# Optimization experiments

Hardware: AMD Instinct MI355X
Metric: run time of the kernel (lower is better)

## Reference

```python
import jax, jax.numpy as jnp
import numpy as np

TOP_RATIO = 0.7
MIN_PATCHES = 128
RANDOM_RATIO = 0.1


def setup_inputs() -> dict:
    key = jax.random.key(0)
    k1, k2, k3, k4 = jax.random.split(key, 4)
    B, N, D, H = 4, 16384, 512, 256
    features = jax.random.normal(k1, (B, N, D), dtype=jnp.float32)
    W_V = jax.random.normal(k2, (D, H), dtype=jnp.float32) * (1.0 / np.sqrt(D))
    W_U = jax.random.normal(k3, (D, H), dtype=jnp.float32) * (1.0 / np.sqrt(D))
    w_att = jax.random.normal(k4, (H,), dtype=jnp.float32) * (1.0 / np.sqrt(H))
    return {
        "features": features,
        "W_V": W_V, "b_V": jnp.zeros((H,), jnp.float32),
        "W_U": W_U, "b_U": jnp.zeros((H,), jnp.float32),
        "w_att": w_att, "b_att": jnp.zeros((), jnp.float32),
    }


def reference(features, W_V, b_V, W_U, b_U, w_att, b_att):
    B, N, D = features.shape
    # gated attention scoring (dropout disabled: eval mode)
    a_V = jnp.tanh(features @ W_V + b_V)              # (B, N, H)
    a_U = jax.nn.sigmoid(features @ W_U + b_U)        # (B, N, H)
    raw = (a_V * a_U) @ w_att + b_att                 # (B, N)
    attn = jax.nn.softmax(raw, axis=-1)               # (B, N)

    # static selection sizes
    k = min(max(int(N * TOP_RATIO), MIN_PATCHES), N)  # 11468
    n_rand = max(int(k * RANDOM_RATIO), 1)            # 1146
    n_top = k - n_rand                                # 10322

    # batched top-k (softmax is monotone in raw, same indices as torch.topk(attn))
    _, top_idx = jax.lax.top_k(attn, n_top)           # (B, n_top)

    # remaining = indices not in top_idx, ascending; fixed count N - n_top
    mask = jnp.ones((B, N), bool).at[jnp.arange(B)[:, None], top_idx].set(False)
    remaining = jnp.argsort(~mask, axis=-1, stable=True)[:, : N - n_top]  # (B, N-n_top)

    # uniform random sample of n_rand remaining indices per batch element
    scores = jax.random.uniform(jax.random.key(42), (B, N - n_top))
    perm = jnp.argsort(scores, axis=-1)[:, :n_rand]   # random n_rand positions
    rand_idx = jnp.take_along_axis(remaining, perm, axis=-1)  # (B, n_rand)

    sel_idx = jnp.sort(jnp.concatenate([top_idx, rand_idx], axis=-1), axis=-1)  # (B, k)
    selected = jnp.take_along_axis(features, sel_idx[:, :, None], axis=1)       # (B, k, D)
    return selected, attn, sel_idx
```

## Files before the change

kernel.cpp:

```cpp
#include <hip/hip_runtime.h>
#include <stdint.h>

#define B 4
#define N 16384
#define D 512
#define H 256
#define NROWS (B * N)
#define K_SEL 11468
#define N_TOP 10322
#define N_RAND 1146
#define N_REM (N - N_TOP)
#define HALF_CNT ((B * N_REM) / 2)

typedef float f32x4 __attribute__((ext_vector_type(4)));
typedef _Float16 f16x8 __attribute__((ext_vector_type(8)));
typedef int i32x4 __attribute__((ext_vector_type(4)));

#define GLDS16(g, l)                                                    \
  __builtin_amdgcn_global_load_lds(                                     \
      (const __attribute__((address_space(1))) void*)(const void*)(g),  \
      (__attribute__((address_space(3))) void*)(void*)(l), 16, 0, 0)

__device__ __forceinline__ uint32_t f2key(float x) {
  uint32_t u = __float_as_uint(x);
  return u ^ ((u & 0x80000000u) ? 0xFFFFFFFFu : 0x80000000u);
}

__device__ __forceinline__ void threefry(uint32_t x0, uint32_t x1,
                                         uint32_t& o0, uint32_t& o1) {
  const uint32_t k0 = 0u, k1 = 42u;
  const uint32_t ks[3] = {k0, k1, k0 ^ k1 ^ 0x1BD11BDAu};
  x0 += ks[0];
  x1 += ks[1];
  const int R0[4] = {13, 15, 26, 6}, R1[4] = {17, 29, 16, 24};
#pragma unroll
  for (int i = 0; i < 5; ++i) {
    const int* R = (i & 1) ? R1 : R0;
#pragma unroll
    for (int jr = 0; jr < 4; ++jr) {
      x0 += x1;
      x1 = (x1 << R[jr]) | (x1 >> (32 - R[jr]));
      x1 ^= x0;
    }
    x0 += ks[(i + 1) % 3];
    x1 += ks[(i + 2) % 3] + (uint32_t)(i + 1);
  }
  o0 = x0;
  o1 = x1;
}

__device__ __forceinline__ void rand_body(const int b, int* __restrict__ psel,
                                          char* smem, const int t) {
  uint32_t* skey = reinterpret_cast<uint32_t*>(smem);
  uint32_t* hist = reinterpret_cast<uint32_t*>(smem + 24248);
  int* wr4 = reinterpret_cast<int*>(smem + 25272);
  uint32_t* shp = reinterpret_cast<uint32_t*>(smem + 25288);
  int* shrk = reinterpret_cast<int*>(smem + 25292);
  const int lane = t & 63, w4 = t >> 6;

  for (int p = t; p < N_REM; p += 256) {
    psel[b * N_REM + p] = 0;
    const int f = b * N_REM + p;
    uint32_t o0, o1, bits;
    if (f < HALF_CNT) {
      threefry((uint32_t)f, (uint32_t)(f + HALF_CNT), o0, o1);
      bits = o0;
    } else {
      threefry((uint32_t)(f - HALF_CNT), (uint32_t)f, o0, o1);
      bits = o1;
    }
    const float u = __uint_as_float((bits >> 9) | 0x3f800000u) - 1.0f;
    skey[p] = f2key(u);
  }
  __syncthreads();

  uint32_t prefix = 0;
  int rk = N_RAND;
  for (int pass = 3; pass >= 0; --pass) {
    const int sh = pass * 8;
    hist[t] = 0;
    __syncthreads();
    for (int p = t; p < N_REM; p += 256) {
      const uint32_t key = skey[p];
      if (pass == 3 || (key >> (sh + 8)) == (prefix >> (sh + 8)))
        atomicAdd(&hist[(key >> sh) & 255], 1u);
    }
    __syncthreads();
    const int h = (int)hist[t];
    int v = h;
#pragma unroll
    for (int off = 1; off < 64; off <<= 1) {
      const int u2 = __shfl_up(v, off, 64);
      if (lane >= off) v += u2;
    }
    if (lane == 63) wr4[w4] = v;
    __syncthreads();
    int add = 0;
    for (int i = 0; i < w4; ++i) add += wr4[i];
    const int incl = v + add, excl = incl - h;
    if (incl >= rk && excl < rk) {
      *shp = prefix | ((uint32_t)t << sh);
      *shrk = rk - excl;
    }
    __syncthreads();
    prefix = *shp;
    rk = *shrk;
    __syncthreads();
  }

  const int CH = 24;
  const int p0 = t * CH;
  const int pe = (p0 + CH < N_REM) ? p0 + CH : N_REM;
  int ce = 0;
  for (int p = p0; p < pe; ++p) ce += (skey[p] == prefix);
  int v = ce;
#pragma unroll
  for (int off = 1; off < 64; off <<= 1) {
    const int u2 = __shfl_up(v, off, 64);
    if (lane >= off) v += u2;
  }
  if (lane == 63) wr4[w4] = v;
  __syncthreads();
  if (t == 0) {
    int run = 0;
    for (int i = 0; i < 4; ++i) {
      const int a = wr4[i];
      wr4[i] = run;
      run += a;
    }
  }
  __syncthreads();
  int ge = wr4[w4] + v - ce;
  for (int p = p0; p < pe; ++p) {
    const uint32_t key = skey[p];
    const bool pick = (key < prefix) || (key == prefix && ge < rk);
    ge += (key == prefix);
    if (pick) psel[b * N_REM + p] = 1;
  }
}

__global__ __launch_bounds__(256) void prep_kernel(
    const float* __restrict__ WV, const float* __restrict__ WU,
    _Float16* __restrict__ wt_h, _Float16* __restrict__ wt_l,
    int* __restrict__ psel) {
  __shared__ __align__(16) char pmem[25296];
  if (blockIdx.x >= 64) {
    rand_body(blockIdx.x - 64, psel, pmem, threadIdx.x);
    return;
  }
  _Float16(*th)[65] = reinterpret_cast<_Float16(*)[65]>(pmem);
  _Float16(*tl)[65] = reinterpret_cast<_Float16(*)[65]>(pmem + 8320);
  const int kb = (blockIdx.x >> 3) * 64;
  const int nb = (blockIdx.x & 7) * 64;
  const int tx = threadIdx.x & 63;
  const int ty = threadIdx.x >> 6;
  const float* src = (nb < 256) ? WV : WU;
  const int nsrc = nb & 255;
#pragma unroll
  for (int i = 0; i < 16; ++i) {
    const int k = ty + i * 4;
    const float x = src[(size_t)(kb + k) * H + nsrc + tx];
    const _Float16 h = (_Float16)x;
    th[k][tx] = h;
    tl[k][tx] = (_Float16)(x - (float)h);
  }
  __syncthreads();
  const int n_local = threadIdx.x & 63;
  const int c2 = threadIdx.x >> 6;
  const int s_local = c2 >> 1, half = c2 & 1;
  const int n = nb + n_local;
  const int s = (kb >> 5) + s_local;
  const int klb = s_local * 32 + half * 16;
  const int swz = (n_local >> 1) & 3;
  f16x8 vh0, vh1, vl0, vl1;
#pragma unroll
  for (int e = 0; e < 8; ++e) {
    vh0[e] = th[klb + e][n_local];
    vh1[e] = th[klb + 8 + e][n_local];
    vl0[e] = tl[klb + e][n_local];
    vl1[e] = tl[klb + 8 + e][n_local];
  }
  const size_t orow = (size_t)s * 16384 + (size_t)n * 32;
  *reinterpret_cast<f16x8*>(wt_h + orow + (((2 * half) ^ swz) * 8)) = vh0;
  *reinterpret_cast<f16x8*>(wt_h + orow + (((2 * half + 1) ^ swz) * 8)) = vh1;
  *reinterpret_cast<f16x8*>(wt_l + orow + (((2 * half) ^ swz) * 8)) = vl0;
  *reinterpret_cast<f16x8*>(wt_l + orow + (((2 * half + 1) ^ swz) * 8)) = vl1;
}

__global__ __launch_bounds__(512) void score_kernel(
    const float* __restrict__ feat, const _Float16* __restrict__ wt_h,
    const _Float16* __restrict__ wt_l, const float* __restrict__ bV,
    const float* __restrict__ bU, const float* __restrict__ watt,
    float* __restrict__ raw) {
  __shared__ _Float16 Ah[128 * 32];
  __shared__ _Float16 Al[128 * 32];
  __shared__ _Float16 Bh0[512 * 32];
  __shared__ _Float16 Bl0[512 * 32];
  __shared__ _Float16 Bh1[512 * 32];
  __shared__ _Float16 Bl1[512 * 32];
  __shared__ float red[128][5];

  const int tid = threadIdx.x;
  const int lane = tid & 63;
  const int lc = lane & 15;
  const int lg = lane >> 4;
  const int w = __builtin_amdgcn_readfirstlane(tid >> 6);
  const int rg = w >> 2;
  const int cg = w & 3;
  const int row0 = blockIdx.x * 128;

  const int rA = tid >> 2;
  const int gA = tid & 3;
  const float* aG = feat + (size_t)(row0 + rA) * D + gA * 8;
  const int awOff = rA * 32 + ((gA ^ ((rA >> 1) & 3)) << 3);

  const _Float16* pbh = wt_h + (size_t)w * 2048 + lane * 8;
  const _Float16* pbl = wt_l + (size_t)w * 2048 + lane * 8;
  const int ldsB = w * 2048;

  const int rswz = (lc >> 1) & 3;
  int aoff[4], boff[8];
#pragma unroll
  for (int mt = 0; mt < 4; ++mt)
    aoff[mt] = (rg * 64 + mt * 16 + lc) * 32 + ((lg ^ rswz) << 3);
#pragma unroll
  for (int nt = 0; nt < 8; ++nt) {
    const int nbase =
        (nt < 4) ? cg * 64 + nt * 16 : 256 + cg * 64 + (nt - 4) * 16;
    boff[nt] = (nbase + lc) * 32 + ((lg ^ rswz) << 3);
  }

  f32x4 acc[4][8] = {};
  f32x4 a0, a1;

  a0 = *(const f32x4*)(aG);
  a1 = *(const f32x4*)(aG + 4);
#pragma unroll
  for (int i = 0; i < 4; ++i) {
    GLDS16(pbh + i * 512, &Bh0[ldsB + i * 512]);
    GLDS16(pbl + i * 512, &Bl0[ldsB + i * 512]);
  }
  {
    f16x8 ahw, alw;
#pragma unroll
    for (int e = 0; e < 8; ++e) {
      const float x = (e < 4) ? a0[e] : a1[e - 4];
      const _Float16 h = (_Float16)x;
      ahw[e] = h;
      alw[e] = (_Float16)(x - (float)h);
    }
    *(f16x8*)&Ah[awOff] = ahw;
    *(f16x8*)&Al[awOff] = alw;
  }
  __syncthreads();

#pragma unroll 1
  for (int kt = 0; kt < 16; ++kt) {
    const int knx = (kt + 1) & 15;
    _Float16* BhN = (kt & 1) ? Bh0 : Bh1;
    _Float16* BlN = (kt & 1) ? Bl0 : Bl1;
    const _Float16* BhC = (kt & 1) ? Bh1 : Bh0;
    const _Float16* BlC = (kt & 1) ? Bl1 : Bl0;

#pragma unroll
    for (int i = 0; i < 4; ++i) {
      GLDS16(pbh + knx * 16384 + i * 512, &BhN[ldsB + i * 512]);
      GLDS16(pbl + knx * 16384 + i * 512, &BlN[ldsB + i * 512]);
    }
    a0 = *(const f32x4*)(aG + knx * 32);
    a1 = *(const f32x4*)(aG + knx * 32 + 4);
    __builtin_amdgcn_sched_barrier(0);

    f16x8 ah[4], al[4];
#pragma unroll
    for (int mt = 0; mt < 4; ++mt) {
      ah[mt] = *(const f16x8*)&Ah[aoff[mt]];
      al[mt] = *(const f16x8*)&Al[aoff[mt]];
    }
    f16x8 bh = *(const f16x8*)&BhC[boff[0]];
    f16x8 bl = *(const f16x8*)&BlC[boff[0]];
    __builtin_amdgcn_s_setprio(1);
#pragma unroll
    for (int nt = 0; nt < 8; ++nt) {
      f16x8 bhn, bln;
      if (nt < 7) {
        bhn = *(const f16x8*)&BhC[boff[nt + 1]];
        bln = *(const f16x8*)&BlC[boff[nt + 1]];
      }
#pragma unroll
      for (int mt = 0; mt < 4; ++mt) {
        acc[mt][nt] = __builtin_amdgcn_mfma_f32_16x16x32_f16(ah[mt], bh,
                                                             acc[mt][nt], 0, 0, 0);
        acc[mt][nt] = __builtin_amdgcn_mfma_f32_16x16x32_f16(ah[mt], bl,
                                                             acc[mt][nt], 0, 0, 0);
        acc[mt][nt] = __builtin_amdgcn_mfma_f32_16x16x32_f16(al[mt], bh,
                                                             acc[mt][nt], 0, 0, 0);
      }
      bh = bhn;
      bl = bln;
    }
    __builtin_amdgcn_s_setprio(0);

    f16x8 ahw, alw;
#pragma unroll
    for (int e = 0; e < 8; ++e) {
      const float x = (e < 4) ? a0[e] : a1[e - 4];
      const _Float16 h = (_Float16)x;
      ahw[e] = h;
      alw[e] = (_Float16)(x - (float)h);
    }
    __syncthreads();
    *(f16x8*)&Ah[awOff] = ahw;
    *(f16x8*)&Al[awOff] = alw;
    __syncthreads();
  }

#pragma unroll
  for (int mt = 0; mt < 4; ++mt) {
    float rs[4] = {0.f, 0.f, 0.f, 0.f};
#pragma unroll
    for (int nt = 0; nt < 4; ++nt) {
      const int j = cg * 64 + nt * 16 + lc;
      const float bv = bV[j], bu = bU[j], wa = watt[j];
#pragma unroll
      for (int rr = 0; rr < 4; ++rr) {
        const float cV = acc[mt][nt][rr] + bv;
        const float cU = acc[mt][nt + 4][rr] + bu;
        const float e2 = __expf(2.0f * cV);
        const float aV = 1.0f - 2.0f / (e2 + 1.0f);
        const float aU = 1.0f / (1.0f + __expf(-cU));
        rs[rr] += aV * aU * wa;
      }
    }
#pragma unroll
    for (int rr = 0; rr < 4; ++rr) {
      float v = rs[rr];
      v += __shfl_xor(v, 1, 16);
      v += __shfl_xor(v, 2, 16);
      v += __shfl_xor(v, 4, 16);
      v += __shfl_xor(v, 8, 16);
      if (lc == 0) red[rg * 64 + mt * 16 + lg * 4 + rr][cg] = v;
    }
  }
  __syncthreads();
  if (tid < 128)
    raw[row0 + tid] = red[tid][0] + red[tid][1] + red[tid][2] + red[tid][3];
}

__device__ __forceinline__ int scan1024(int c, int* wred, int tid) {
  const int lane = tid & 63, w = tid >> 6;
  int v = c;
#pragma unroll
  for (int off = 1; off < 64; off <<= 1) {
    const int u = __shfl_up(v, off, 64);
    if (lane >= off) v += u;
  }
  if (lane == 63) wred[w] = v;
  __syncthreads();
  if (tid == 0) {
    int run = 0;
    for (int i = 0; i < 16; ++i) {
      const int a = wred[i];
      wred[i] = run;
      run += a;
    }
  }
  __syncthreads();
  const int res = wred[w] + v - c;
  __syncthreads();
  return res;
}

__global__ __launch_bounds__(1024) void select_kernel(
    const float* __restrict__ raw, const int* __restrict__ psel,
    float* __restrict__ attn_out, int* __restrict__ sel_ws,
    float* __restrict__ out_selidx) {
  const int b = blockIdx.x, t = threadIdx.x;
  const int lane = t & 63, w = t >> 6;
  __shared__ float sraw[N];
  __shared__ int whist[16][256];
  __shared__ int ghist[256];
  __shared__ float fred[16];
  __shared__ int wred[16];
  __shared__ float shM, shS;
  __shared__ uint32_t sh_prefix;
  __shared__ int sh_rk;
  const float* r = raw + b * N;

  float m = -3.0e38f;
  for (int i = 0; i < 16; ++i) {
    const int idx = t + i * 1024;
    const float v = r[idx];
    sraw[idx] = v;
    m = fmaxf(m, v);
  }
  for (int off = 32; off > 0; off >>= 1) m = fmaxf(m, __shfl_down(m, off, 64));
  if (lane == 0) fred[w] = m;
  __syncthreads();
  if (t == 0) {
    float mm = fred[0];
    for (int i = 1; i < 16; ++i) mm = fmaxf(mm, fred[i]);
    shM = mm;
  }
  __syncthreads();
  const float M = shM;

  float ex[16];
  float s = 0.f;
  for (int i = 0; i < 16; ++i) {
    ex[i] = expf(sraw[t + i * 1024] - M);
    s += ex[i];
  }
  for (int off = 32; off > 0; off >>= 1) s += __shfl_down(s, off, 64);
  if (lane == 0) fred[w] = s;
  __syncthreads();
  if (t == 0) {
    float ss = 0.f;
    for (int i = 0; i < 16; ++i) ss += fred[i];
    shS = ss;
  }
  __syncthreads();
  const float inv = 1.0f / shS;

  for (int i = 0; i < 16; ++i)
    attn_out[b * N + t + i * 1024] = ex[i] * inv;

  uint32_t prefix = 0;
  int rk = N_TOP;
  for (int pass = 3; pass >= 0; --pass) {
    const int sh = pass * 8;
#pragma unroll
    for (int q = 0; q < 4; ++q) whist[w][lane * 4 + q] = 0;
    __syncthreads();
    for (int i = 0; i < 16; ++i) {
      const uint32_t key = f2key(sraw[t + i * 1024]);
      if (pass == 3 || (key >> (sh + 8)) == (prefix >> (sh + 8)))
        atomicAdd(&whist[w][(key >> sh) & 255], 1);
    }
    __syncthreads();
    if (t < 256) {
      int tot = 0;
      for (int ww = 0; ww < 16; ++ww) tot += whist[ww][t];
      ghist[t] = tot;
    }
    __syncthreads();
    int vS = 0, hrev = 0;
    if (t < 256) {
      hrev = ghist[255 - t];
      vS = hrev;
#pragma unroll
      for (int off = 1; off < 64; off <<= 1) {
        const int u2 = __shfl_up(vS, off, 64);
        if (lane >= off) vS += u2;
      }
      if (lane == 63) wred[t >> 6] = vS;
    }
    __syncthreads();
    if (t < 256) {
      int add = 0;
      const int w4 = t >> 6;
      for (int i = 0; i < w4; ++i) add += wred[i];
      const int incl = vS + add, excl = incl - hrev;
      if (incl >= rk && excl < rk) {
        sh_prefix = prefix | ((uint32_t)(255 - t) << sh);
        sh_rk = rk - excl;
      }
    }
    __syncthreads();
    prefix = sh_prefix;
    rk = sh_rk;
    __syncthreads();
  }
  const uint32_t T = prefix;
  const int tieTake = rk;

  const int n0 = t * 16;
  int cgt = 0, ceq = 0;
  for (int i = 0; i < 16; ++i) {
    const uint32_t key = f2key(sraw[n0 + i]);
    cgt += (key > T);
    ceq += (key == T);
  }
  const int gbase = scan1024(cgt, wred, t);
  const int ebase = scan1024(ceq, wred, t);
  int grun = gbase, erun = ebase;
  unsigned selmask = 0;
  int csel = 0;
  for (int i = 0; i < 16; ++i) {
    const int n = n0 + i;
    const uint32_t key = f2key(sraw[n]);
    const bool gt = key > T, eq = key == T;
    const bool mem = gt || (eq && erun < tieTake);
    int sel;
    if (mem) {
      sel = 1;
    } else {
      const int members_before = grun + (erun < tieTake ? erun : tieTake);
      const int p = n - members_before;
      sel = psel[b * N_REM + p];
    }
    selmask |= (unsigned)sel << i;
    csel += sel;
    grun += gt;
    erun += eq;
  }
  int q = scan1024(csel, wred, t);
  for (int i = 0; i < 16; ++i) {
    if ((selmask >> i) & 1) {
      const int n = n0 + i;
      sel_ws[b * K_SEL + q] = n;
      out_selidx[b * K_SEL + q] = (float)n;
      ++q;
    }
  }
}

__global__ __launch_bounds__(128) void gather_kernel(
    const float* __restrict__ feat, const int* __restrict__ sel_ws,
    float* __restrict__ out_sel) {
  const int qa = blockIdx.x;
  const int b = qa / K_SEL;
  const int n = sel_ws[qa];
  const float4* src =
      reinterpret_cast<const float4*>(feat + (size_t)(b * N + n) * D);
  float4* dst = reinterpret_cast<float4*>(out_sel + (size_t)qa * D);
  dst[threadIdx.x] = src[threadIdx.x];
}

extern "C" void kernel_launch(void* const* d_in, const int* in_sizes, int n_in,
                              void* d_out, int out_size, void* d_ws,
                              size_t ws_size, hipStream_t stream) {
  const float* feat = (const float*)d_in[0];
  const float* WV = (const float*)d_in[1];
  const float* bV = (const float*)d_in[2];
  const float* WU = (const float*)d_in[3];
  const float* bU = (const float*)d_in[4];
  const float* watt = (const float*)d_in[5];
  const float* batt = (const float*)d_in[6];
  (void)batt;

  float* out = (float*)d_out;
  float* out_selected = out;
  float* out_attn = out + (size_t)B * K_SEL * D;
  float* out_selidx = out_attn + (size_t)B * N;

  _Float16* wt_h = (_Float16*)d_ws;
  _Float16* wt_l = wt_h + 512 * 512;
  float* raw = (float*)(wt_l + 512 * 512);
  int* psel = (int*)(raw + NROWS);
  int* sel_ws = psel + B * N_REM;

  prep_kernel<<<68, 256, 0, stream>>>(WV, WU, wt_h, wt_l, psel);
  score_kernel<<<NROWS / 128, 512, 0, stream>>>(feat, wt_h, wt_l, bV, bU, watt,
                                                raw);
  select_kernel<<<B, 1024, 0, stream>>>(raw, psel, out_attn, sel_ws,
                                        out_selidx);
  gather_kernel<<<B * K_SEL, 128, 0, stream>>>(feat, sel_ws, out_selected);
}
```

Baseline: 351.4 us.

## Split score GEMM across two column-half blocks with partial raw outputs

The score kernel now launches twice as many blocks. Each block handles 128 rows but only half of the hidden columns (128 of the V and the matching 128 of the U). The prep kernel relays out the weights into per-chunk groups, and each block writes a partial raw score to its own buffer. The select kernel sums the two partials. This halves LDS and accumulator usage per block, which raises occupancy (launch bounds now request 4 blocks) and the number of blocks in flight, at the cost of reading the feature tiles twice and doing the fp16 split conversion twice.

```diff
diff --git a/kernel.cpp b/kernel.cpp
--- a/kernel.cpp
+++ b/kernel.cpp
@@ -171,7 +171,10 @@
   const int n = nb + n_local;
   const int s = (kb >> 5) + s_local;
   const int klb = s_local * 32 + half * 16;
-  const int swz = (n_local >> 1) & 3;
+  const int j = (n < 256) ? n : n - 256;
+  const int ch = j >> 7;
+  const int nl = ((n < 256) ? 0 : 128) + (j & 127);
+  const int swz = (nl >> 1) & 3;
   f16x8 vh0, vh1, vl0, vl1;
 #pragma unroll
   for (int e = 0; e < 8; ++e) {
@@ -180,25 +183,25 @@
     vl0[e] = tl[klb + e][n_local];
     vl1[e] = tl[klb + 8 + e][n_local];
   }
-  const size_t orow = (size_t)s * 16384 + (size_t)n * 32;
+  const size_t orow = (size_t)s * 16384 + (size_t)ch * 8192 + (size_t)nl * 32;
   *reinterpret_cast<f16x8*>(wt_h + orow + (((2 * half) ^ swz) * 8)) = vh0;
   *reinterpret_cast<f16x8*>(wt_h + orow + (((2 * half + 1) ^ swz) * 8)) = vh1;
   *reinterpret_cast<f16x8*>(wt_l + orow + (((2 * half) ^ swz) * 8)) = vl0;
   *reinterpret_cast<f16x8*>(wt_l + orow + (((2 * half + 1) ^ swz) * 8)) = vl1;
 }
 
-__global__ __launch_bounds__(512) void score_kernel(
+__global__ __launch_bounds__(512, 4) void score_kernel(
     const float* __restrict__ feat, const _Float16* __restrict__ wt_h,
     const _Float16* __restrict__ wt_l, const float* __restrict__ bV,
     const float* __restrict__ bU, const float* __restrict__ watt,
-    float* __restrict__ raw) {
+    float* __restrict__ rawp) {
   __shared__ _Float16 Ah[128 * 32];
   __shared__ _Float16 Al[128 * 32];
-  __shared__ _Float16 Bh0[512 * 32];
-  __shared__ _Float16 Bl0[512 * 32];
-  __shared__ _Float16 Bh1[512 * 32];
-  __shared__ _Float16 Bl1[512 * 32];
-  __shared__ float red[128][5];
+  __shared__ _Float16 Bh0[256 * 32];
+  __shared__ _Float16 Bl0[256 * 32];
+  __shared__ _Float16 Bh1[256 * 32];
+  __shared__ _Float16 Bl1[256 * 32];
+  float* red = reinterpret_cast<float*>(Ah);
 
   const int tid = threadIdx.x;
   const int lane = tid & 63;
@@ -207,39 +210,40 @@
   const int w = __builtin_amdgcn_readfirstlane(tid >> 6);
   const int rg = w >> 2;
   const int cg = w & 3;
-  const int row0 = blockIdx.x * 128;
+  const int bid = blockIdx.x;
+  const int c = bid & 1;
+  const int row0 = (bid >> 1) * 128;
 
   const int rA = tid >> 2;
   const int gA = tid & 3;
   const float* aG = feat + (size_t)(row0 + rA) * D + gA * 8;
   const int awOff = rA * 32 + ((gA ^ ((rA >> 1) & 3)) << 3);
 
-  const _Float16* pbh = wt_h + (size_t)w * 2048 + lane * 8;
-  const _Float16* pbl = wt_l + (size_t)w * 2048 + lane * 8;
-  const int ldsB = w * 2048;
+  const _Float16* pbh = wt_h + (size_t)c * 8192 + (size_t)w * 1024 + lane * 8;
+  const _Float16* pbl = wt_l + (size_t)c * 8192 + (size_t)w * 1024 + lane * 8;
+  const int ldsB = w * 1024;
 
   const int rswz = (lc >> 1) & 3;
-  int aoff[4], boff[8];
+  int aoff[4], boff[4];
 #pragma unroll
   for (int mt = 0; mt < 4; ++mt)
     aoff[mt] = (rg * 64 + mt * 16 + lc) * 32 + ((lg ^ rswz) << 3);
 #pragma unroll
-  for (int nt = 0; nt < 8; ++nt) {
-    const int nbase =
-        (nt < 4) ? cg * 64 + nt * 16 : 256 + cg * 64 + (nt - 4) * 16;
-    boff[nt] = (nbase + lc) * 32 + ((lg ^ rswz) << 3);
-  }
-
-  f32x4 acc[4][8] = {};
+  for (int nt = 0; nt < 4; ++nt) {
+    const int nl =
+        ((nt < 2) ? cg * 32 + nt * 16 : 128 + cg * 32 + (nt - 2) * 16) + lc;
+    boff[nt] = nl * 32 + ((lg ^ rswz) << 3);
+  }
+
+  f32x4 acc[4][4] = {};
   f32x4 a0, a1;
 
   a0 = *(const f32x4*)(aG);
   a1 = *(const f32x4*)(aG + 4);
-#pragma unroll
-  for (int i = 0; i < 4; ++i) {
-    GLDS16(pbh + i * 512, &Bh0[ldsB + i * 512]);
-    GLDS16(pbl + i * 512, &Bl0[ldsB + i * 512]);
-  }
+  GLDS16(pbh, &Bh0[ldsB]);
+  GLDS16(pbh + 512, &Bh0[ldsB + 512]);
+  GLDS16(pbl, &Bl0[ldsB]);
+  GLDS16(pbl + 512, &Bl0[ldsB + 512]);
   {
     f16x8 ahw, alw;
 #pragma unroll
@@ -262,11 +266,10 @@
     const _Float16* BhC = (kt & 1) ? Bh1 : Bh0;
     const _Float16* BlC = (kt & 1) ? Bl1 : Bl0;
 
-#pragma unroll
-    for (int i = 0; i < 4; ++i) {
-      GLDS16(pbh + knx * 16384 + i * 512, &BhN[ldsB + i * 512]);
-      GLDS16(pbl + knx * 16384 + i * 512, &BlN[ldsB + i * 512]);
-    }
+    GLDS16(pbh + knx * 16384, &BhN[ldsB]);
+    GLDS16(pbh + knx * 16384 + 512, &BhN[ldsB + 512]);
+    GLDS16(pbl + knx * 16384, &BlN[ldsB]);
+    GLDS16(pbl + knx * 16384 + 512, &BlN[ldsB + 512]);
     a0 = *(const f32x4*)(aG + knx * 32);
     a1 = *(const f32x4*)(aG + knx * 32 + 4);
     __builtin_amdgcn_sched_barrier(0);
@@ -277,16 +280,11 @@
       ah[mt] = *(const f16x8*)&Ah[aoff[mt]];
       al[mt] = *(const f16x8*)&Al[aoff[mt]];
     }
-    f16x8 bh = *(const f16x8*)&BhC[boff[0]];
-    f16x8 bl = *(const f16x8*)&BlC[boff[0]];
     __builtin_amdgcn_s_setprio(1);
 #pragma unroll
-    for (int nt = 0; nt < 8; ++nt) {
-      f16x8 bhn, bln;
-      if (nt < 7) {
-        bhn = *(const f16x8*)&BhC[boff[nt + 1]];
-        bln = *(const f16x8*)&BlC[boff[nt + 1]];
-      }
+    for (int nt = 0; nt < 4; ++nt) {
+      const f16x8 bh = *(const f16x8*)&BhC[boff[nt]];
+      const f16x8 bl = *(const f16x8*)&BlC[boff[nt]];
 #pragma unroll
       for (int mt = 0; mt < 4; ++mt) {
         acc[mt][nt] = __builtin_amdgcn_mfma_f32_16x16x32_f16(ah[mt], bh,
@@ -296,8 +294,6 @@
         acc[mt][nt] = __builtin_amdgcn_mfma_f32_16x16x32_f16(al[mt], bh,
                                                              acc[mt][nt], 0, 0, 0);
       }
-      bh = bhn;
-      bl = bln;
     }
     __builtin_amdgcn_s_setprio(0);
 
@@ -319,13 +315,13 @@
   for (int mt = 0; mt < 4; ++mt) {
     float rs[4] = {0.f, 0.f, 0.f, 0.f};
 #pragma unroll
-    for (int nt = 0; nt < 4; ++nt) {
-      const int j = cg * 64 + nt * 16 + lc;
+    for (int nt = 0; nt < 2; ++nt) {
+      const int j = c * 128 + cg * 32 + nt * 16 + lc;
       const float bv = bV[j], bu = bU[j], wa = watt[j];
 #pragma unroll
       for (int rr = 0; rr < 4; ++rr) {
         const float cV = acc[mt][nt][rr] + bv;
-        const float cU = acc[mt][nt + 4][rr] + bu;
+        const float cU = acc[mt][nt + 2][rr] + bu;
         const float e2 = __expf(2.0f * cV);
         const float aV = 1.0f - 2.0f / (e2 + 1.0f);
         const float aU = 1.0f / (1.0f + __expf(-cU));
@@ -339,12 +335,13 @@
       v += __shfl_xor(v, 2, 16);
       v += __shfl_xor(v, 4, 16);
       v += __shfl_xor(v, 8, 16);
-      if (lc == 0) red[rg * 64 + mt * 16 + lg * 4 + rr][cg] = v;
+      if (lc == 0) red[(rg * 64 + mt * 16 + lg * 4 + rr) * 5 + cg] = v;
     }
   }
   __syncthreads();
   if (tid < 128)
-    raw[row0 + tid] = red[tid][0] + red[tid][1] + red[tid][2] + red[tid][3];
+    rawp[(size_t)c * NROWS + row0 + tid] = red[tid * 5 + 0] + red[tid * 5 + 1] +
+                                           red[tid * 5 + 2] + red[tid * 5 + 3];
 }
 
 __device__ __forceinline__ int scan1024(int c, int* wred, int tid) {
@@ -372,7 +369,7 @@
 }
 
 __global__ __launch_bounds__(1024) void select_kernel(
-    const float* __restrict__ raw, const int* __restrict__ psel,
+    const float* __restrict__ rawp, const int* __restrict__ psel,
     float* __restrict__ attn_out, int* __restrict__ sel_ws,
     float* __restrict__ out_selidx) {
   const int b = blockIdx.x, t = threadIdx.x;
@@ -385,12 +382,13 @@
   __shared__ float shM, shS;
   __shared__ uint32_t sh_prefix;
   __shared__ int sh_rk;
-  const float* r = raw + b * N;
+  const float* r0 = rawp + (size_t)b * N;
+  const float* r1 = rawp + (size_t)NROWS + b * N;
 
   float m = -3.0e38f;
   for (int i = 0; i < 16; ++i) {
     const int idx = t + i * 1024;
-    const float v = r[idx];
+    const float v = r0[idx] + r1[idx];
     sraw[idx] = v;
     m = fmaxf(m, v);
   }
@@ -546,14 +544,14 @@
 
   _Float16* wt_h = (_Float16*)d_ws;
   _Float16* wt_l = wt_h + 512 * 512;
-  float* raw = (float*)(wt_l + 512 * 512);
-  int* psel = (int*)(raw + NROWS);
+  float* rawp = (float*)(wt_l + 512 * 512);
+  int* psel = (int*)(rawp + 2 * NROWS);
   int* sel_ws = psel + B * N_REM;
 
   prep_kernel<<<68, 256, 0, stream>>>(WV, WU, wt_h, wt_l, psel);
-  score_kernel<<<NROWS / 128, 512, 0, stream>>>(feat, wt_h, wt_l, bV, bU, watt,
-                                                raw);
-  select_kernel<<<B, 1024, 0, stream>>>(raw, psel, out_attn, sel_ws,
+  score_kernel<<<(NROWS / 128) * 2, 512, 0, stream>>>(feat, wt_h, wt_l, bV, bU,
+                                                      watt, rawp);
+  select_kernel<<<B, 1024, 0, stream>>>(rawp, psel, out_attn, sel_ws,
                                         out_selidx);
   gather_kernel<<<B * K_SEL, 128, 0, stream>>>(feat, sel_ws, out_selected);
 }
```

Measured after the change: 342.5 us. 1.03x faster.
